# Performance work log

Hardware: AMD Instinct MI355X
Metric: run time of the kernel (lower is better)

The kernel has to match this reference:

```python
import jax, jax.numpy as jnp
import numpy as np

B, C, PC, P = 64, 32, 128, 2048
N = B * C * PC          # 262144 graph nodes
E = 2097152             # ~8 edges per node


def _gcn(x, src, dst, n, W, b):
    # PyG GCNConv: add self loops, sym-normalized mean aggregation of x@W
    xw = x @ W
    sl = jnp.arange(n, dtype=src.dtype)
    s = jnp.concatenate([src, sl]); d = jnp.concatenate([dst, sl])
    deg = jax.ops.segment_sum(jnp.ones(d.shape, xw.dtype), d, num_segments=n)
    dinv = jax.lax.rsqrt(deg)  # deg >= 1 thanks to self loops
    norm = dinv[s] * dinv[d]
    return jax.ops.segment_sum(xw[s] * norm[:, None], d, num_segments=n) + b


def _gat(x, src, dst, n, W, a_src, a_dst, b):
    # PyG GATConv (heads=1): self loops, edge softmax over incoming edges
    xw = x @ W
    sl = jnp.arange(n, dtype=src.dtype)
    s = jnp.concatenate([src, sl]); d = jnp.concatenate([dst, sl])
    e = jax.nn.leaky_relu((xw @ a_src)[s] + (xw @ a_dst)[d], 0.2)
    m = jax.ops.segment_max(jax.lax.stop_gradient(e), d, num_segments=n)
    ex = jnp.exp(e - m[d])
    denom = jax.ops.segment_sum(ex, d, num_segments=n)
    alpha = ex / denom[d]
    return jax.ops.segment_sum(xw[s] * alpha[:, None], d, num_segments=n) + b


def _cross_edges(num_cross, batch_size):
    # faithful to get_c_adjacency: every ordered pair (i!=j) appears twice per graph
    ii, jj = np.meshgrid(np.arange(num_cross), np.arange(num_cross), indexing='ij')
    m = ii != jj
    s, d = ii[m], jj[m]
    s2 = np.concatenate([s, d]); d2 = np.concatenate([d, s])
    off = (np.arange(batch_size) * num_cross)[:, None]
    src = (s2[None] + off).reshape(-1)
    dst = (d2[None] + off).reshape(-1)
    return jnp.asarray(src, jnp.int32), jnp.asarray(dst, jnp.int32)


def _conv1d(x, W, b):
    y = jax.lax.conv_general_dilated(x, W, (2,), ((1, 1),), dimension_numbers=('NCH', 'OIH', 'NCH'))
    return y + b[None, :, None]


def _bn_eval(x, gamma, beta):
    # BatchNorm1d in eval mode with default running stats (mean 0, var 1)
    scale = gamma / np.float32(np.sqrt(1.0 + 1e-5))
    return x * scale[None, :, None] + beta[None, :, None]


def setup_inputs() -> dict:
    key = jax.random.key(0)
    ks = jax.random.split(key, 32)
    rn = lambda k, sh, s=0.1: (jax.random.normal(k, sh, jnp.float32) * s)
    return {
        'x': jax.random.normal(ks[0], (N, 19), jnp.float32),
        'edge_index': jax.random.randint(ks[1], (2, E), 0, N, jnp.int32),
        'points': jax.random.normal(ks[2], (B, 3, P), jnp.float32),
        'W1': rn(ks[3], (19, 32)), 'b1': rn(ks[4], (32,)),
        'W2': rn(ks[5], (32, 64)), 'b2': rn(ks[6], (64,)),
        'W3': rn(ks[7], (64, 64)), 'b3': rn(ks[8], (64,)),
        'Wg1': rn(ks[9], (64, 64)), 'asrc1': rn(ks[10], (64,)), 'adst1': rn(ks[11], (64,)), 'bg1': rn(ks[12], (64,)),
        'Wg2': rn(ks[13], (64, 64)), 'asrc2': rn(ks[14], (64,)), 'adst2': rn(ks[15], (64,)), 'bg2': rn(ks[16], (64,)),
        'c1W': rn(ks[17], (32, 3, 3)), 'c1b': rn(ks[18], (32,)),
        'g1': 1.0 + rn(ks[19], (32,)), 'be1': rn(ks[20], (32,)),
        'c2W': rn(ks[21], (64, 32, 3)), 'c2b': rn(ks[22], (64,)),
        'g2': 1.0 + rn(ks[23], (64,)), 'be2': rn(ks[24], (64,)),
        'c3W': rn(ks[25], (64, 64, 3)), 'c3b': rn(ks[26], (64,)),
        'Wl2': rn(ks[27], (64, 64)), 'bl2': rn(ks[28], (64,)),
        'Wl3': rn(ks[29], (64, 1)), 'bl3': rn(ks[30], (1,)),
        'batch_size': B, 'num_cross': C, 'num_pieces': PC,
    }


def reference(x, edge_index, points, W1, b1, W2, b2, W3, b3,
              Wg1, asrc1, adst1, bg1, Wg2, asrc2, adst2, bg2,
              c1W, c1b, g1, be1, c2W, c2b, g2, be2, c3W, c3b,
              Wl2, bl2, Wl3, bl3, batch_size, num_cross, num_pieces):
    src, dst = edge_index[0], edge_index[1]
    n = x.shape[0]
    h = jax.nn.relu(_gcn(x, src, dst, n, W1, b1))  # dropout is a no-op in eval
    h = jax.nn.leaky_relu(_gcn(h, src, dst, n, W2, b2), 0.01)
    h = jax.nn.leaky_relu(_gcn(h, src, dst, n, W3, b3), 0.01)
    h = _gat(h, src, dst, n, Wg1, asrc1, adst1, bg1)
    h = h.reshape(batch_size, num_cross, num_pieces, -1).mean(-2)  # [B, C, 64]
    s2, d2 = _cross_edges(num_cross, batch_size)
    h = _gat(h.reshape(batch_size * num_cross, 64), s2, d2, batch_size * num_cross, Wg2, asrc2, adst2, bg2)
    h = h.reshape(batch_size, num_cross, 64).mean(1)  # [B, 64]
    p = _bn_eval(jax.nn.leaky_relu(_conv1d(points, c1W, c1b), 0.01), g1, be1)
    p = _bn_eval(jax.nn.leaky_relu(_conv1d(p, c2W, c2b), 0.01), g2, be2)
    p = jax.nn.leaky_relu(_conv1d(p, c3W, c3b), 0.01).mean(-1)  # AdaptiveAvgPool1d(1).squeeze -> [B, 64]
    h = h + p
    h = jax.nn.leaky_relu(h @ Wl2 + bl2, 0.01)
    return jax.nn.sigmoid(h @ Wl3 + bl3)  # [B, 1]
```

## Files before the change

### kernel.cpp

```cpp
#include <hip/hip_runtime.h>
#include <cstdint>
#include <cstddef>

#define NN 262144
#define EE 2097152
#define BB 64
#define CCROSS 32
#define PCC 128
#define PP 2048
#define NBUCK 256
#define BCAP 12288

typedef _Float16 f16;
typedef __attribute__((ext_vector_type(2))) _Float16 f16x2;
typedef __attribute__((ext_vector_type(4))) _Float16 f16x4;
typedef __attribute__((ext_vector_type(8))) _Float16 f16x8;
typedef __attribute__((ext_vector_type(4))) float f32x4;

static __device__ __forceinline__ float lrelu(float x, float s) { return x > 0.f ? x : s * x; }

#if __has_builtin(__builtin_amdgcn_fdot2)
static __device__ __forceinline__ float dot2f(unsigned x, unsigned w, float c) {
    return __builtin_amdgcn_fdot2(__builtin_bit_cast(f16x2, x), __builtin_bit_cast(f16x2, w), c, false);
}
#else
static __device__ __forceinline__ float dot2f(unsigned x, unsigned w, float c) {
    f16x2 a = __builtin_bit_cast(f16x2, x);
    f16x2 b = __builtin_bit_cast(f16x2, w);
    return fmaf((float)a[0], (float)b[0], fmaf((float)a[1], (float)b[1], c));
}
#endif

__global__ __launch_bounds__(256) void bucket_a_k(const int* __restrict__ src, const int* __restrict__ dst,
                                                  unsigned* __restrict__ buckets, int* __restrict__ gcnt) {
    __shared__ int hist[NBUCK];
    __shared__ int base[NBUCK];
    __shared__ unsigned short rankbuf[8192];
    const int tid = threadIdx.x;
    const int e0 = blockIdx.x * 8192;
    hist[tid] = 0;
    __syncthreads();
    for (int i = tid; i < 8192; i += 256) {
        int d = dst[e0 + i];
        rankbuf[i] = (unsigned short)atomicAdd(&hist[d >> 10], 1);
    }
    __syncthreads();
    base[tid] = tid * BCAP + atomicAdd(&gcnt[tid], hist[tid]);
    __syncthreads();
    for (int i = tid; i < 8192; i += 256) {
        int s = src[e0 + i];
        int d = dst[e0 + i];
        int b = d >> 10;
        buckets[base[b] + rankbuf[i]] = ((unsigned)s << 10) | (unsigned)(d & 1023);
    }
}

__global__ void bucket_scan_k(const int* __restrict__ gcnt, int* __restrict__ bbase, int* __restrict__ rp) {
    __shared__ int tmp[256];
    int tid = threadIdx.x;
    int v = gcnt[tid];
    tmp[tid] = v;
    __syncthreads();
    for (int off = 1; off < 256; off <<= 1) {
        int t = (tid >= off) ? tmp[tid - off] : 0;
        __syncthreads();
        tmp[tid] += t;
        __syncthreads();
    }
    bbase[tid] = tmp[tid] - v;
    if (tid == 0) rp[NN] = EE;
}

__global__ __launch_bounds__(256) void bucket_b_k(const unsigned* __restrict__ buckets, const int* __restrict__ gcnt,
                                                  const int* __restrict__ bbase, int* __restrict__ rp,
                                                  float* __restrict__ dinv, int* __restrict__ col) {
    __shared__ int cnt[1024];
    __shared__ int scan[1024];
    __shared__ int wsum[256];
    const int b = blockIdx.x;
    const int tid = threadIdx.x;
    int n = gcnt[b];
    if (n > BCAP) n = BCAP;
    const unsigned* eb = buckets + (size_t)b * BCAP;
    const int gb = bbase[b];
    for (int i = tid; i < 1024; i += 256) cnt[i] = 0;
    __syncthreads();
    for (int i = tid; i < n; i += 256) atomicAdd(&cnt[eb[i] & 1023], 1);
    __syncthreads();
    int b4 = tid * 4;
    int c0 = cnt[b4], c1 = cnt[b4 + 1], c2 = cnt[b4 + 2], c3 = cnt[b4 + 3];
    int tsum = c0 + c1 + c2 + c3;
    wsum[tid] = tsum;
    __syncthreads();
    for (int off = 1; off < 256; off <<= 1) {
        int t = (tid >= off) ? wsum[tid - off] : 0;
        __syncthreads();
        wsum[tid] += t;
        __syncthreads();
    }
    int excl = wsum[tid] - tsum;
    scan[b4] = excl;
    scan[b4 + 1] = excl + c0;
    scan[b4 + 2] = excl + c0 + c1;
    scan[b4 + 3] = excl + c0 + c1 + c2;
    int vbase = b * 1024 + b4;
    rp[vbase + 0] = gb + scan[b4 + 0];
    rp[vbase + 1] = gb + scan[b4 + 1];
    rp[vbase + 2] = gb + scan[b4 + 2];
    rp[vbase + 3] = gb + scan[b4 + 3];
    dinv[vbase + 0] = rsqrtf((float)(c0 + 1));
    dinv[vbase + 1] = rsqrtf((float)(c1 + 1));
    dinv[vbase + 2] = rsqrtf((float)(c2 + 1));
    dinv[vbase + 3] = rsqrtf((float)(c3 + 1));
    __syncthreads();
    for (int i = tid; i < 1024; i += 256) cnt[i] = 0;
    __syncthreads();
    for (int i = tid; i < n; i += 256) {
        unsigned p = eb[i];
        int dl = p & 1023;
        int r = atomicAdd(&cnt[dl], 1);
        col[gb + scan[dl] + r] = (int)(p >> 10);
    }
}

__global__ void zprep_k(const float* __restrict__ x, const float* __restrict__ dinv, f16* __restrict__ z) {
    int v = blockIdx.x * 256 + threadIdx.x;
    if (v >= NN) return;
    float dv = dinv[v];
    const float* xr = x + (size_t)v * 19;
    float vv[20];
#pragma unroll
    for (int k = 0; k < 19; k++) vv[k] = dv * xr[k];
    vv[19] = 0.f;
    f16x4* zr = (f16x4*)(z + (size_t)v * 32);
#pragma unroll
    for (int c = 0; c < 5; c++) {
        f16x4 t = {(f16)vv[4 * c], (f16)vv[4 * c + 1], (f16)vv[4 * c + 2], (f16)vv[4 * c + 3]};
        zr[c] = t;
    }
    f16x4 zz = {(f16)0.f, (f16)0.f, (f16)0.f, (f16)0.f};
#pragma unroll
    for (int c = 5; c < 8; c++) zr[c] = zz;
}

#define ZSTR1 36
template <int KINR, int KOUT, int ACT>
__global__ __launch_bounds__(256) void fused_agg_gemm_k(const f16* __restrict__ z, const int* __restrict__ rp,
                                                        const int* __restrict__ col, const float* __restrict__ Wg,
                                                        const float* __restrict__ dinv, const float* __restrict__ bias,
                                                        f16* __restrict__ zout) {
    constexpr int NO = KOUT / 4;
    __shared__ float Wl[32 * KOUT];
    __shared__ float zrow[64 * ZSTR1];
    const int tid = threadIdx.x;
    for (int i = tid; i < 32 * KOUT; i += 256) Wl[i] = (i < KINR * KOUT) ? Wg[i] : 0.f;

    const int r = tid >> 2;
    const int idx = tid & 3;
    const int v = blockIdx.x * 64 + r;
    const f16x8* z8 = (const f16x8*)z;
    f16x8 a = z8[(size_t)v * 4 + idx];
    float acc8[8];
#pragma unroll
    for (int j = 0; j < 8; j++) acc8[j] = (float)a[j];
    int st = rp[v], e = rp[v + 1];
    int i = st;
    for (; i + 4 <= e; i += 4) {
        int u0 = col[i], u1 = col[i + 1], u2 = col[i + 2], u3 = col[i + 3];
        f16x8 a0 = z8[(size_t)u0 * 4 + idx];
        f16x8 a1 = z8[(size_t)u1 * 4 + idx];
        f16x8 a2 = z8[(size_t)u2 * 4 + idx];
        f16x8 a3 = z8[(size_t)u3 * 4 + idx];
#pragma unroll
        for (int j = 0; j < 8; j++)
            acc8[j] += ((float)a0[j] + (float)a1[j]) + ((float)a2[j] + (float)a3[j]);
    }
    for (; i < e; i++) {
        f16x8 aa = z8[(size_t)col[i] * 4 + idx];
#pragma unroll
        for (int j = 0; j < 8; j++) acc8[j] += (float)aa[j];
    }
    float4 s0, s1;
    s0.x = acc8[0]; s0.y = acc8[1]; s0.z = acc8[2]; s0.w = acc8[3];
    s1.x = acc8[4]; s1.y = acc8[5]; s1.z = acc8[6]; s1.w = acc8[7];
    *(float4*)&zrow[r * ZSTR1 + idx * 8] = s0;
    *(float4*)&zrow[r * ZSTR1 + idx * 8 + 4] = s1;
    __syncthreads();

    float acc[NO];
#pragma unroll
    for (int j = 0; j < NO; j++) acc[j] = 0.f;
#pragma unroll 4
    for (int k = 0; k < 32; k++) {
        float zv = zrow[r * ZSTR1 + k];
        const float* wr = Wl + k * KOUT + NO * idx;
#pragma unroll
        for (int j = 0; j < NO; j++) acc[j] = fmaf(zv, wr[j], acc[j]);
    }
    float dv = dinv[v];
    f16 hv[NO];
#pragma unroll
    for (int j = 0; j < NO; j++) {
        float o = dv * acc[j] + bias[NO * idx + j];
        o = (ACT == 0) ? fmaxf(o, 0.f) : lrelu(o, 0.01f);
        hv[j] = (f16)(o * dv);
    }
    if constexpr (NO == 8) {
        f16x8 h = {hv[0], hv[1], hv[2], hv[3], hv[4], hv[5], hv[6], hv[7]};
        *(f16x8*)(zout + (size_t)v * KOUT + NO * idx) = h;
    } else {
        f16x8 h0 = {hv[0], hv[1], hv[2], hv[3], hv[4], hv[5], hv[6], hv[7]};
        f16x8 h1 = {hv[8], hv[9], hv[10], hv[11], hv[12], hv[13], hv[14], hv[15]};
        f16x8* yo = (f16x8*)(zout + (size_t)v * KOUT + NO * idx);
        yo[0] = h0; yo[1] = h1;
    }
}

__global__ __launch_bounds__(256) void agg_h16_k(const f16* __restrict__ y, const int* __restrict__ rp,
                                                 const int* __restrict__ col, f16* __restrict__ out) {
    int gid = blockIdx.x * 256 + threadIdx.x;
    int v = gid >> 3;
    int idx = gid & 7;
    const f16x8* y8 = (const f16x8*)y;
    f16x8 a = y8[(size_t)v * 8 + idx];
    float acc[8];
#pragma unroll
    for (int j = 0; j < 8; j++) acc[j] = (float)a[j];
    int s = rp[v], e = rp[v + 1];
    int i = s;
    for (; i + 4 <= e; i += 4) {
        int u0 = col[i], u1 = col[i + 1], u2 = col[i + 2], u3 = col[i + 3];
        f16x8 a0 = y8[(size_t)u0 * 8 + idx];
        f16x8 a1 = y8[(size_t)u1 * 8 + idx];
        f16x8 a2 = y8[(size_t)u2 * 8 + idx];
        f16x8 a3 = y8[(size_t)u3 * 8 + idx];
#pragma unroll
        for (int j = 0; j < 8; j++)
            acc[j] += ((float)a0[j] + (float)a1[j]) + ((float)a2[j] + (float)a3[j]);
    }
    for (; i < e; i++) {
        f16x8 aa = y8[(size_t)col[i] * 8 + idx];
#pragma unroll
        for (int j = 0; j < 8; j++) acc[j] += (float)aa[j];
    }
    f16x8 r;
#pragma unroll
    for (int j = 0; j < 8; j++) r[j] = (f16)acc[j];
    ((f16x8*)out)[(size_t)v * 8 + idx] = r;
}

__global__ void pack_w_k(const float* __restrict__ W, f16* __restrict__ out) {
    int o = blockIdx.x * 256 + threadIdx.x;
    if (o >= 4096) return;
    int frag = o >> 9;
    int kt = frag >> 2;
    int c = frag & 3;
    int idx = o & 511;
    int l = idx >> 3;
    int j = idx & 7;
    int k = kt * 32 + ((l >> 4) << 3) + j;
    int n = 16 * c + (l & 15);
    out[o] = (f16)W[k * 64 + n];
}

__global__ void pack_c2_k(const float* __restrict__ W, f16* __restrict__ out) {
    int o = blockIdx.x * 256 + threadIdx.x;
    if (o >= 64 * 96) return;
    int ch = o / 96, r = o - ch * 96;
    int k = r >> 5, ci = r & 31;
    out[o] = (f16)W[ch * 96 + ci * 3 + k];
}

__global__ void pack_c3_k(const float* __restrict__ W, f16* __restrict__ out) {
    int o = blockIdx.x * 256 + threadIdx.x;
    if (o >= 64 * 192) return;
    int ch = o / 192, r = o - ch * 192;
    int k = r >> 6, ci = r & 63;
    out[o] = (f16)W[ch * 192 + ci * 3 + k];
}

#define HSTR 72
__global__ __launch_bounds__(256) void gemm3_gat_k(const f16* __restrict__ aggz, const f16* __restrict__ w3p,
                                                   const float* __restrict__ dinv, const float* __restrict__ b3,
                                                   const f16* __restrict__ wgp, const float* __restrict__ av,
                                                   const float* __restrict__ ad, f16* __restrict__ xw,
                                                   float* __restrict__ es, float* __restrict__ ed) {
    __shared__ f16 zin[64 * HSTR];
    __shared__ f16 hh[64 * HSTR];
    const int tid = threadIdx.x;
    const int v0 = blockIdx.x * 64;
    {
        int row = tid >> 2;
        int kb = (tid & 3) * 16;
        const f16x8* zp = (const f16x8*)(aggz + (size_t)(v0 + row) * 64 + kb);
        f16x8 z0 = zp[0], z1 = zp[1];
        *(f16x8*)&zin[row * HSTR + kb] = z0;
        *(f16x8*)&zin[row * HSTR + kb + 8] = z1;
    }
    __syncthreads();

    const int w = tid >> 6;
    const int l = tid & 63;
    const int m = l & 15;
    const int q = l >> 4;
    const int r0 = 16 * w;

    f32x4 acc0 = {0.f, 0.f, 0.f, 0.f}, acc1 = acc0, acc2 = acc0, acc3 = acc0;
#pragma unroll
    for (int kt = 0; kt < 2; kt++) {
        f16x8 afrag = *(const f16x8*)&zin[(r0 + m) * HSTR + kt * 32 + q * 8];
        f16x8 b0 = *(const f16x8*)&w3p[((kt * 4 + 0) << 9) + l * 8];
        f16x8 b1 = *(const f16x8*)&w3p[((kt * 4 + 1) << 9) + l * 8];
        f16x8 b2 = *(const f16x8*)&w3p[((kt * 4 + 2) << 9) + l * 8];
        f16x8 b3f = *(const f16x8*)&w3p[((kt * 4 + 3) << 9) + l * 8];
        acc0 = __builtin_amdgcn_mfma_f32_16x16x32_f16(afrag, b0, acc0, 0, 0, 0);
        acc1 = __builtin_amdgcn_mfma_f32_16x16x32_f16(afrag, b1, acc1, 0, 0, 0);
        acc2 = __builtin_amdgcn_mfma_f32_16x16x32_f16(afrag, b2, acc2, 0, 0, 0);
        acc3 = __builtin_amdgcn_mfma_f32_16x16x32_f16(afrag, b3f, acc3, 0, 0, 0);
    }
    {
        float dv0 = dinv[v0 + r0 + q * 4 + 0];
        float dv1 = dinv[v0 + r0 + q * 4 + 1];
        float dv2 = dinv[v0 + r0 + q * 4 + 2];
        float dv3 = dinv[v0 + r0 + q * 4 + 3];
#pragma unroll
        for (int c = 0; c < 4; c++) {
            const f32x4* ac = (c == 0) ? &acc0 : (c == 1) ? &acc1 : (c == 2) ? &acc2 : &acc3;
            float bb = b3[16 * c + m];
            hh[(r0 + q * 4 + 0) * HSTR + 16 * c + m] = (f16)lrelu(dv0 * (*ac)[0] + bb, 0.01f);
            hh[(r0 + q * 4 + 1) * HSTR + 16 * c + m] = (f16)lrelu(dv1 * (*ac)[1] + bb, 0.01f);
            hh[(r0 + q * 4 + 2) * HSTR + 16 * c + m] = (f16)lrelu(dv2 * (*ac)[2] + bb, 0.01f);
            hh[(r0 + q * 4 + 3) * HSTR + 16 * c + m] = (f16)lrelu(dv3 * (*ac)[3] + bb, 0.01f);
        }
    }
    __syncthreads();

    acc0 = (f32x4){0.f, 0.f, 0.f, 0.f}; acc1 = acc0; acc2 = acc0; acc3 = acc0;
#pragma unroll
    for (int kt = 0; kt < 2; kt++) {
        f16x8 afrag = *(const f16x8*)&hh[(r0 + m) * HSTR + kt * 32 + q * 8];
        f16x8 b0 = *(const f16x8*)&wgp[((kt * 4 + 0) << 9) + l * 8];
        f16x8 b1 = *(const f16x8*)&wgp[((kt * 4 + 1) << 9) + l * 8];
        f16x8 b2 = *(const f16x8*)&wgp[((kt * 4 + 2) << 9) + l * 8];
        f16x8 b3f = *(const f16x8*)&wgp[((kt * 4 + 3) << 9) + l * 8];
        acc0 = __builtin_amdgcn_mfma_f32_16x16x32_f16(afrag, b0, acc0, 0, 0, 0);
        acc1 = __builtin_amdgcn_mfma_f32_16x16x32_f16(afrag, b1, acc1, 0, 0, 0);
        acc2 = __builtin_amdgcn_mfma_f32_16x16x32_f16(afrag, b2, acc2, 0, 0, 0);
        acc3 = __builtin_amdgcn_mfma_f32_16x16x32_f16(afrag, b3f, acc3, 0, 0, 0);
    }
    {
        float e1[4] = {0.f, 0.f, 0.f, 0.f}, e2[4] = {0.f, 0.f, 0.f, 0.f};
#pragma unroll
        for (int c = 0; c < 4; c++) {
            const f32x4* ac = (c == 0) ? &acc0 : (c == 1) ? &acc1 : (c == 2) ? &acc2 : &acc3;
            float a1 = av[16 * c + m];
            float d1 = ad[16 * c + m];
#pragma unroll
            for (int reg = 0; reg < 4; reg++) {
                float g = (*ac)[reg];
                e1[reg] = fmaf(g, a1, e1[reg]);
                e2[reg] = fmaf(g, d1, e2[reg]);
                xw[(size_t)(v0 + r0 + q * 4 + reg) * 64 + 16 * c + m] = (f16)g;
            }
        }
#pragma unroll
        for (int reg = 0; reg < 4; reg++) {
            e1[reg] += __shfl_xor(e1[reg], 1); e1[reg] += __shfl_xor(e1[reg], 2);
            e1[reg] += __shfl_xor(e1[reg], 4); e1[reg] += __shfl_xor(e1[reg], 8);
            e2[reg] += __shfl_xor(e2[reg], 1); e2[reg] += __shfl_xor(e2[reg], 2);
            e2[reg] += __shfl_xor(e2[reg], 4); e2[reg] += __shfl_xor(e2[reg], 8);
        }
        if (m == 0) {
#pragma unroll
            for (int reg = 0; reg < 4; reg++) {
                es[v0 + r0 + q * 4 + reg] = e1[reg];
                ed[v0 + r0 + q * 4 + reg] = e2[reg];
            }
        }
    }
}

__global__ void gat_w_k(const float* __restrict__ es, const float* __restrict__ ed,
                        const int* __restrict__ rp, const int* __restrict__ col,
                        f16* __restrict__ ew, float* __restrict__ wself, float* __restrict__ invden) {
    int v = blockIdx.x * 256 + threadIdx.x;
    if (v >= NN) return;
    float edv = ed[v];
    float eself = lrelu(es[v] + edv, 0.2f);
    float m = eself;
    int s = rp[v], e = rp[v + 1];
    int i = s;
    float lg[32];
    for (; i + 4 <= e; i += 4) {
        int u0 = col[i], u1 = col[i + 1], u2 = col[i + 2], u3 = col[i + 3];
        float t0 = lrelu(es[u0] + edv, 0.2f);
        float t1 = lrelu(es[u1] + edv, 0.2f);
        float t2 = lrelu(es[u2] + edv, 0.2f);
        float t3 = lrelu(es[u3] + edv, 0.2f);
        int k = i - s;
        if (k + 3 < 32) { lg[k] = t0; lg[k + 1] = t1; lg[k + 2] = t2; lg[k + 3] = t3; }
        m = fmaxf(m, fmaxf(fmaxf(t0, t1), fmaxf(t2, t3)));
    }
    for (; i < e; i++) {
        float t = lrelu(es[col[i]] + edv, 0.2f);
        int k = i - s;
        if (k < 32) lg[k] = t;
        m = fmaxf(m, t);
    }
    float wsl = __expf(eself - m);
    float den = wsl;
    for (i = s; i < e; i++) {
        int k = i - s;
        float t = (k < 32) ? lg[k] : lrelu(es[col[i]] + edv, 0.2f);
        float w = __expf(t - m);
        ew[i] = (f16)w;
        den += w;
    }
    wself[v] = wsl;
    invden[v] = 1.f / den;
}

__global__ __launch_bounds__(256) void gat_agg_pool_k(const f16* __restrict__ y, const int* __restrict__ rp,
                                                      const int* __restrict__ col, const f16* __restrict__ ew,
                                                      const float* __restrict__ wself, const float* __restrict__ invden,
                                                      const float* __restrict__ bias, float* __restrict__ pooled) {
    __shared__ float sred[32 * 68];
    const int g = blockIdx.x;
    const int tid = threadIdx.x;
    const int idx = tid & 7;
    const int slot = tid >> 3;
    const f16x8* y8 = (const f16x8*)y;
    float pacc[8];
#pragma unroll
    for (int j = 0; j < 8; j++) pacc[j] = 0.f;

#pragma unroll 1
    for (int pass = 0; pass < 4; pass++) {
        const int v = g * 128 + pass * 32 + slot;
        float ws = wself[v];
        f16x8 self = y8[(size_t)v * 8 + idx];
        float acc[8];
#pragma unroll
        for (int j = 0; j < 8; j++) acc[j] = ws * (float)self[j];
        int s = rp[v], e = rp[v + 1];
        int i = s;
        for (; i + 4 <= e; i += 4) {
            int u0 = col[i], u1 = col[i + 1], u2 = col[i + 2], u3 = col[i + 3];
            float w0 = (float)ew[i], w1 = (float)ew[i + 1], w2 = (float)ew[i + 2], w3 = (float)ew[i + 3];
            f16x8 a0 = y8[(size_t)u0 * 8 + idx];
            f16x8 a1 = y8[(size_t)u1 * 8 + idx];
            f16x8 a2 = y8[(size_t)u2 * 8 + idx];
            f16x8 a3 = y8[(size_t)u3 * 8 + idx];
#pragma unroll
            for (int j = 0; j < 8; j++)
                acc[j] = fmaf(w0, (float)a0[j], fmaf(w1, (float)a1[j], fmaf(w2, (float)a2[j], fmaf(w3, (float)a3[j], acc[j]))));
        }
        for (; i < e; i++) {
            float w = (float)ew[i];
            f16x8 aa = y8[(size_t)col[i] * 8 + idx];
#pragma unroll
            for (int j = 0; j < 8; j++) acc[j] = fmaf(w, (float)aa[j], acc[j]);
        }
        float inv = invden[v];
#pragma unroll
        for (int j = 0; j < 8; j++) pacc[j] = fmaf(acc[j], inv, pacc[j]);
    }

#pragma unroll
    for (int j = 0; j < 8; j++) sred[slot * 68 + idx * 8 + j] = pacc[j];
    __syncthreads();
    if (tid < 64) {
        float s = 0.f;
#pragma unroll
        for (int k = 0; k < 32; k++) s += sred[k * 68 + tid];
        pooled[(size_t)g * 64 + tid] = s * (1.f / 128.f) + bias[tid];
    }
}

__global__ void pool_cross_k(const float* __restrict__ in, float* __restrict__ out) {
    int gid = blockIdx.x * 64 + threadIdx.x;
    if (gid >= BB * 64) return;
    int f = gid & 63, b = gid >> 6;
    const float* p = in + (size_t)b * CCROSS * 64 + f;
    float s = 0.f;
#pragma unroll
    for (int i = 0; i < CCROSS; i++) s += p[(size_t)i * 64];
    out[gid] = s * (1.f / 32.f);
}

template <int KIN, int KOUT>
__global__ void gat_gemm_k(const float* __restrict__ x, const float* __restrict__ W,
                           float* __restrict__ y, const float* __restrict__ av, const float* __restrict__ ad,
                           float* __restrict__ es, float* __restrict__ ed, int n) {
    int v = blockIdx.x * 256 + threadIdx.x;
    if (v >= n) return;
    const float* xr = x + (size_t)v * KIN;
    float acc[KOUT];
#pragma unroll
    for (int j = 0; j < KOUT; j++) acc[j] = 0.f;
#pragma unroll 2
    for (int k = 0; k < KIN; k++) {
        float xv = xr[k];
#pragma unroll
        for (int j = 0; j < KOUT; j++) acc[j] = fmaf(xv, W[k * KOUT + j], acc[j]);
    }
    float e1 = 0.f, e2 = 0.f;
    float4* y4 = (float4*)(y + (size_t)v * KOUT);
#pragma unroll
    for (int j4 = 0; j4 < KOUT / 4; j4++) {
        float4 t;
        t.x = acc[4 * j4 + 0]; t.y = acc[4 * j4 + 1]; t.z = acc[4 * j4 + 2]; t.w = acc[4 * j4 + 3];
        y4[j4] = t;
        e1 = fmaf(t.x, av[4 * j4 + 0], e1); e1 = fmaf(t.y, av[4 * j4 + 1], e1);
        e1 = fmaf(t.z, av[4 * j4 + 2], e1); e1 = fmaf(t.w, av[4 * j4 + 3], e1);
        e2 = fmaf(t.x, ad[4 * j4 + 0], e2); e2 = fmaf(t.y, ad[4 * j4 + 1], e2);
        e2 = fmaf(t.z, ad[4 * j4 + 2], e2); e2 = fmaf(t.w, ad[4 * j4 + 3], e2);
    }
    es[v] = e1; ed[v] = e2;
}

__global__ void cross_att_k(const float* __restrict__ xw, const float* __restrict__ es,
                            const float* __restrict__ ed, const float* __restrict__ bg,
                            float* __restrict__ out) {
    int gid = blockIdx.x * 256 + threadIdx.x;
    if (gid >= BB * CCROSS * 64) return;
    int f = gid & 63;
    int d = (gid >> 6) & 31;
    int g = gid >> 11;
    int base = g * CCROSS;
    float edd = ed[base + d];
    float m = -1e30f;
#pragma unroll
    for (int s = 0; s < CCROSS; s++) {
        float e = lrelu(es[base + s] + edd, 0.2f);
        m = fmaxf(m, e);
    }
    float den = 0.f, acc = 0.f;
#pragma unroll
    for (int s = 0; s < CCROSS; s++) {
        float e = lrelu(es[base + s] + edd, 0.2f);
        float w = __expf(e - m) * ((s == d) ? 1.f : 2.f);
        den += w;
        acc = fmaf(w, xw[(size_t)(base + s) * 64 + f], acc);
    }
    out[gid] = acc / den + bg[f];
}

__global__ __launch_bounds__(256) void conv_fused_k(
        const float* __restrict__ pts, const float* __restrict__ c1W, const float* __restrict__ c1b,
        const float* __restrict__ g1, const float* __restrict__ be1,
        const f16* __restrict__ w2p, const float* __restrict__ c2b,
        const float* __restrict__ g2, const float* __restrict__ be2,
        const f16* __restrict__ w3pc, const float* __restrict__ c3b,
        float* __restrict__ partials) {
    __shared__ __align__(16) float s0[3 * 264];
    __shared__ __align__(16) f16 s1T[132 * 32];
    __shared__ __align__(16) f16 s2T[66 * 64];
    __shared__ float sred[256];

    const int b = blockIdx.x >> 3;
    const int q = blockIdx.x & 7;
    const int tid = threadIdx.x;
    const float bnscale = 0.99999500003749968f;

    const int lo0 = 256 * q - 7;
    for (int t = tid; t < 3 * 263; t += 256) {
        int c = t / 263, j = t - c * 263;
        int p = lo0 + j;
        s0[c * 264 + j] = (p >= 0 && p < PP) ? pts[((size_t)b * 3 + c) * PP + p] : 0.f;
    }
    __syncthreads();

    {
        const int ch = tid & 31;
        const int j0 = tid >> 5;
        float wv[9];
        const float* wg = c1W + ch * 9;
#pragma unroll
        for (int t = 0; t < 9; t++) wv[t] = wg[t];
        const float bs = c1b[ch];
        const float gs = g1[ch] * bnscale;
        const float bt = be1[ch];
        const int lo1 = 128 * q - 3;
        for (int j = j0; j < 131; j += 8) {
            int p1 = lo1 + j;
            float v = 0.f;
            if (p1 >= 0 && p1 < 1024) {
                const float* x0 = s0 + 2 * j;
                float a0 = bs, a1 = 0.f, a2 = 0.f;
#pragma unroll
                for (int c = 0; c < 3; c++) {
                    float2 x01 = *(const float2*)(x0 + c * 264);
                    float x2v = x0[c * 264 + 2];
                    a0 = fmaf(x01.x, wv[c * 3 + 0], a0);
                    a1 = fmaf(x01.y, wv[c * 3 + 1], a1);
                    a2 = fmaf(x2v, wv[c * 3 + 2], a2);
                }
                float acc = a0 + a1 + a2;
                acc = lrelu(acc, 0.01f);
                v = fmaf(acc, gs, bt);
            }
            s1T[j * 32 + ch] = (f16)v;
        }
    }
    __syncthreads();

    {
        const int ch = tid & 63;
        const int jg = tid >> 6;
        unsigned wr[48];
        const uint4* wp = (const uint4*)(w2p + (size_t)ch * 96);
#pragma unroll
        for (int t = 0; t < 12; t++) {
            uint4 u = wp[t];
            wr[4 * t + 0] = u.x; wr[4 * t + 1] = u.y; wr[4 * t + 2] = u.z; wr[4 * t + 3] = u.w;
        }
        const float bs = c2b[ch];
        const float gs = g2[ch] * bnscale;
        const float bt = be2[ch];
        const int lo2v = 64 * q - 1;
        for (int j = jg; j < 65; j += 4) {
            float ak[3] = {bs, 0.f, 0.f};
#pragma unroll
            for (int k = 0; k < 3; k++) {
                const uint4* xp = (const uint4*)(s1T + (2 * j + k) * 32);
                uint4 x0 = xp[0], x1 = xp[1], x2 = xp[2], x3 = xp[3];
                float a = ak[k];
                a = dot2f(x0.x, wr[k * 16 + 0], a);
                a = dot2f(x0.y, wr[k * 16 + 1], a);
                a = dot2f(x0.z, wr[k * 16 + 2], a);
                a = dot2f(x0.w, wr[k * 16 + 3], a);
                a = dot2f(x1.x, wr[k * 16 + 4], a);
                a = dot2f(x1.y, wr[k * 16 + 5], a);
                a = dot2f(x1.z, wr[k * 16 + 6], a);
                a = dot2f(x1.w, wr[k * 16 + 7], a);
                a = dot2f(x2.x, wr[k * 16 + 8], a);
                a = dot2f(x2.y, wr[k * 16 + 9], a);
                a = dot2f(x2.z, wr[k * 16 + 10], a);
                a = dot2f(x2.w, wr[k * 16 + 11], a);
                a = dot2f(x3.x, wr[k * 16 + 12], a);
                a = dot2f(x3.y, wr[k * 16 + 13], a);
                a = dot2f(x3.z, wr[k * 16 + 14], a);
                a = dot2f(x3.w, wr[k * 16 + 15], a);
                ak[k] = a;
            }
            float acc = ak[0] + ak[1] + ak[2];
            int p2 = lo2v + j;
            float v = 0.f;
            if (p2 >= 0 && p2 < 512) v = fmaf(lrelu(acc, 0.01f), gs, bt);
            s2T[j * 64 + ch] = (f16)v;
        }
    }
    __syncthreads();

    {
        const int ch = tid & 63;
        const int jg = tid >> 6;
        unsigned wr[96];
        const uint4* wp = (const uint4*)(w3pc + (size_t)ch * 192);
#pragma unroll
        for (int t = 0; t < 24; t++) {
            uint4 u = wp[t];
            wr[4 * t + 0] = u.x; wr[4 * t + 1] = u.y; wr[4 * t + 2] = u.z; wr[4 * t + 3] = u.w;
        }
        const float bs = c3b[ch];
        float psum = 0.f;
        for (int j = jg; j < 32; j += 4) {
            float ak[3] = {bs, 0.f, 0.f};
#pragma unroll
            for (int k = 0; k < 3; k++) {
                const uint4* xp = (const uint4*)(s2T + (2 * j + k) * 64);
                float a = ak[k];
#pragma unroll
                for (int t = 0; t < 8; t++) {
                    uint4 xv = xp[t];
                    a = dot2f(xv.x, wr[k * 32 + 4 * t + 0], a);
                    a = dot2f(xv.y, wr[k * 32 + 4 * t + 1], a);
                    a = dot2f(xv.z, wr[k * 32 + 4 * t + 2], a);
                    a = dot2f(xv.w, wr[k * 32 + 4 * t + 3], a);
                }
                ak[k] = a;
            }
            psum += lrelu(ak[0] + ak[1] + ak[2], 0.01f);
        }
        sred[tid] = psum;
    }
    __syncthreads();
    if (tid < 64) {
        float s = sred[tid] + sred[tid + 64] + sred[tid + 128] + sred[tid + 192];
        partials[((size_t)b * 8 + q) * 64 + tid] = s;
    }
}

__global__ void head_k(const float* __restrict__ hG, const float* __restrict__ partials,
                       const float* __restrict__ Wl2, const float* __restrict__ bl2,
                       const float* __restrict__ Wl3, const float* __restrict__ bl3,
                       float* __restrict__ out) {
    int b = blockIdx.x;
    int f = threadIdx.x;
    __shared__ float sh[64];
    float p = 0.f;
#pragma unroll
    for (int q = 0; q < 8; q++) p += partials[((size_t)b * 8 + q) * 64 + f];
    float h = hG[b * 64 + f] + p * (1.f / 256.f);
    sh[f] = h;
    __syncthreads();
    float acc = bl2[f];
#pragma unroll
    for (int k = 0; k < 64; k++) acc = fmaf(sh[k], Wl2[k * 64 + f], acc);
    acc = lrelu(acc, 0.01f);
    float pr = acc * Wl3[f];
#pragma unroll
    for (int off = 32; off > 0; off >>= 1) pr += __shfl_down(pr, off, 64);
    if (f == 0) out[b] = 1.f / (1.f + __expf(-(pr + bl3[0])));
}

extern "C" void kernel_launch(void* const* d_in, const int* in_sizes, int n_in,
                              void* d_out, int out_size, void* d_ws, size_t ws_size,
                              hipStream_t stream) {
    const float* x = (const float*)d_in[0];
    const int* ei = (const int*)d_in[1];
    const float* points = (const float*)d_in[2];
    const float* W1 = (const float*)d_in[3];
    const float* b1 = (const float*)d_in[4];
    const float* W2 = (const float*)d_in[5];
    const float* b2 = (const float*)d_in[6];
    const float* W3 = (const float*)d_in[7];
    const float* b3 = (const float*)d_in[8];
    const float* Wg1 = (const float*)d_in[9];
    const float* asrc1 = (const float*)d_in[10];
    const float* adst1 = (const float*)d_in[11];
    const float* bg1 = (const float*)d_in[12];
    const float* Wg2 = (const float*)d_in[13];
    const float* asrc2 = (const float*)d_in[14];
    const float* adst2 = (const float*)d_in[15];
    const float* bg2 = (const float*)d_in[16];
    const float* c1W = (const float*)d_in[17];
    const float* c1b = (const float*)d_in[18];
    const float* g1 = (const float*)d_in[19];
    const float* be1 = (const float*)d_in[20];
    const float* c2W = (const float*)d_in[21];
    const float* c2b = (const float*)d_in[22];
    const float* g2 = (const float*)d_in[23];
    const float* be2 = (const float*)d_in[24];
    const float* c3W = (const float*)d_in[25];
    const float* c3b = (const float*)d_in[26];
    const float* Wl2 = (const float*)d_in[27];
    const float* bl2 = (const float*)d_in[28];
    const float* Wl3 = (const float*)d_in[29];
    const float* bl3 = (const float*)d_in[30];

    const int* src = ei;
    const int* dst = ei + EE;

    char* w = (char*)d_ws;
    size_t off = 0;
    auto A = [&](size_t bytes) -> void* {
        void* p = w + off;
        off = (off + bytes + 255) & ~(size_t)255;
        return p;
    };
    int* colb = (int*)A((size_t)EE * 4);
    int* rp = (int*)A((size_t)(NN + 1) * 4);
    int* gcnt = (int*)A(NBUCK * 4);
    int* bbase = (int*)A(NBUCK * 4);
    float* dinv = (float*)A((size_t)NN * 4);
    float* bufA = (float*)A((size_t)NN * 64 * 4);
    f16* bufH1 = (f16*)A((size_t)NN * 64 * 2);
    f16* bufH2 = (f16*)A((size_t)NN * 64 * 2);
    f16* ew = (f16*)A((size_t)EE * 2);
    float* wself = (float*)A((size_t)NN * 4);
    float* invden = (float*)A((size_t)NN * 4);
    float* es = (float*)A((size_t)NN * 4);
    float* edv = (float*)A((size_t)NN * 4);
    f16* w3p = (f16*)A(4096 * 2);
    f16* wgp = (f16*)A(4096 * 2);
    f16* wc2p = (f16*)A(64 * 96 * 2);
    f16* wc3p = (f16*)A(64 * 192 * 2);
    float* pooled = (float*)A((size_t)BB * CCROSS * 64 * 4);
    float* xw2 = (float*)A((size_t)BB * CCROSS * 64 * 4);
    float* es2 = (float*)A((size_t)BB * CCROSS * 4);
    float* ed2 = (float*)A((size_t)BB * CCROSS * 4);
    float* crosso = (float*)A((size_t)BB * CCROSS * 64 * 4);
    float* hG = (float*)A((size_t)BB * 64 * 4);
    float* partials = (float*)A((size_t)BB * 8 * 64 * 4);

    unsigned* buckets = (unsigned*)bufA;
    f16* aggH = (f16*)bufA;

    hipMemsetAsync(gcnt, 0, NBUCK * 4, stream);
    bucket_a_k<<<EE / 8192, 256, 0, stream>>>(src, dst, buckets, gcnt);
    bucket_scan_k<<<1, 256, 0, stream>>>(gcnt, bbase, rp);
    bucket_b_k<<<NBUCK, 256, 0, stream>>>(buckets, gcnt, bbase, rp, dinv, colb);

    pack_c2_k<<<24, 256, 0, stream>>>(c2W, wc2p);
    pack_c3_k<<<48, 256, 0, stream>>>(c3W, wc3p);
    conv_fused_k<<<BB * 8, 256, 0, stream>>>(points, c1W, c1b, g1, be1, wc2p, c2b, g2, be2, wc3p, c3b, partials);
    pack_w_k<<<16, 256, 0, stream>>>(W3, w3p);
    pack_w_k<<<16, 256, 0, stream>>>(Wg1, wgp);

    zprep_k<<<NN / 256, 256, 0, stream>>>(x, dinv, bufH1);
    fused_agg_gemm_k<19, 32, 0><<<NN / 64, 256, 0, stream>>>(bufH1, rp, colb, W1, dinv, b1, bufH2);
    fused_agg_gemm_k<32, 64, 1><<<NN / 64, 256, 0, stream>>>(bufH2, rp, colb, W2, dinv, b2, bufH1);
    agg_h16_k<<<(NN * 8) / 256, 256, 0, stream>>>(bufH1, rp, colb, aggH);
    gemm3_gat_k<<<NN / 64, 256, 0, stream>>>(aggH, w3p, dinv, b3, wgp, asrc1, adst1,
                                             bufH2, es, edv);

    gat_w_k<<<NN / 256, 256, 0, stream>>>(es, edv, rp, colb, ew, wself, invden);
    gat_agg_pool_k<<<BB * CCROSS, 256, 0, stream>>>(bufH2, rp, colb, ew, wself, invden, bg1, pooled);

    gat_gemm_k<64, 64><<<(BB * CCROSS) / 256, 256, 0, stream>>>(pooled, Wg2, xw2, asrc2, adst2, es2, ed2, BB * CCROSS);
    cross_att_k<<<(BB * CCROSS * 64) / 256, 256, 0, stream>>>(xw2, es2, ed2, bg2, crosso);
    pool_cross_k<<<BB, 64, 0, stream>>>(crosso, hG);

    head_k<<<BB, 64, 0, stream>>>(hG, partials, Wl2, bl2, Wl3, bl3, (float*)d_out);
}
```

Measured before the change: 486.8 us.

## Fuse layer-3 aggregation into GEMM and flatten GAT pooling over CSR edges

Folds the standalone layer-3 neighbour aggregation into the gemm3_gat kernel, so each block gathers its 64 rows straight into shared memory. This removes an intermediate NN×64 half-precision write and read plus one kernel launch. GAT weights are now normalized by the softmax denominator inside gat_w_k. That lets gat_agg_pool_k walk the contiguous edge range of a whole 128-node group with strided threads instead of per-node loops, which balances load and removes the per-node invden multiply. The costs are fewer threads per row during the fused gather (4 rather than 8), which limits memory-level parallelism, and an extra pass over edges in gat_w_k.

```diff
diff --git a/kernel.cpp b/kernel.cpp
--- a/kernel.cpp
+++ b/kernel.cpp
@@ -216,39 +216,6 @@
     }
 }
 
-__global__ __launch_bounds__(256) void agg_h16_k(const f16* __restrict__ y, const int* __restrict__ rp,
-                                                 const int* __restrict__ col, f16* __restrict__ out) {
-    int gid = blockIdx.x * 256 + threadIdx.x;
-    int v = gid >> 3;
-    int idx = gid & 7;
-    const f16x8* y8 = (const f16x8*)y;
-    f16x8 a = y8[(size_t)v * 8 + idx];
-    float acc[8];
-#pragma unroll
-    for (int j = 0; j < 8; j++) acc[j] = (float)a[j];
-    int s = rp[v], e = rp[v + 1];
-    int i = s;
-    for (; i + 4 <= e; i += 4) {
-        int u0 = col[i], u1 = col[i + 1], u2 = col[i + 2], u3 = col[i + 3];
-        f16x8 a0 = y8[(size_t)u0 * 8 + idx];
-        f16x8 a1 = y8[(size_t)u1 * 8 + idx];
-        f16x8 a2 = y8[(size_t)u2 * 8 + idx];
-        f16x8 a3 = y8[(size_t)u3 * 8 + idx];
-#pragma unroll
-        for (int j = 0; j < 8; j++)
-            acc[j] += ((float)a0[j] + (float)a1[j]) + ((float)a2[j] + (float)a3[j]);
-    }
-    for (; i < e; i++) {
-        f16x8 aa = y8[(size_t)col[i] * 8 + idx];
-#pragma unroll
-        for (int j = 0; j < 8; j++) acc[j] += (float)aa[j];
-    }
-    f16x8 r;
-#pragma unroll
-    for (int j = 0; j < 8; j++) r[j] = (f16)acc[j];
-    ((f16x8*)out)[(size_t)v * 8 + idx] = r;
-}
-
 __global__ void pack_w_k(const float* __restrict__ W, f16* __restrict__ out) {
     int o = blockIdx.x * 256 + threadIdx.x;
     if (o >= 4096) return;
@@ -280,7 +247,8 @@
 }
 
 #define HSTR 72
-__global__ __launch_bounds__(256) void gemm3_gat_k(const f16* __restrict__ aggz, const f16* __restrict__ w3p,
+__global__ __launch_bounds__(256) void gemm3_gat_k(const f16* __restrict__ y, const int* __restrict__ rp,
+                                                   const int* __restrict__ col, const f16* __restrict__ w3p,
                                                    const float* __restrict__ dinv, const float* __restrict__ b3,
                                                    const f16* __restrict__ wgp, const float* __restrict__ av,
                                                    const float* __restrict__ ad, f16* __restrict__ xw,
@@ -290,12 +258,41 @@
     const int tid = threadIdx.x;
     const int v0 = blockIdx.x * 64;
     {
-        int row = tid >> 2;
-        int kb = (tid & 3) * 16;
-        const f16x8* zp = (const f16x8*)(aggz + (size_t)(v0 + row) * 64 + kb);
-        f16x8 z0 = zp[0], z1 = zp[1];
-        *(f16x8*)&zin[row * HSTR + kb] = z0;
-        *(f16x8*)&zin[row * HSTR + kb + 8] = z1;
+        const int row = tid >> 2;
+        const int idx = tid & 3;
+        const int v = v0 + row;
+        const f16x8* y8 = (const f16x8*)y;
+        f16x8 s0 = y8[(size_t)v * 8 + idx * 2];
+        f16x8 s1 = y8[(size_t)v * 8 + idx * 2 + 1];
+        float acc[16];
+#pragma unroll
+        for (int j = 0; j < 8; j++) { acc[j] = (float)s0[j]; acc[8 + j] = (float)s1[j]; }
+        int s = rp[v], e = rp[v + 1];
+        int i = s;
+        for (; i + 2 <= e; i += 2) {
+            int u0 = col[i], u1 = col[i + 1];
+            f16x8 a0 = y8[(size_t)u0 * 8 + idx * 2];
+            f16x8 a1 = y8[(size_t)u0 * 8 + idx * 2 + 1];
+            f16x8 b0 = y8[(size_t)u1 * 8 + idx * 2];
+            f16x8 b1 = y8[(size_t)u1 * 8 + idx * 2 + 1];
+#pragma unroll
+            for (int j = 0; j < 8; j++) {
+                acc[j] += (float)a0[j] + (float)b0[j];
+                acc[8 + j] += (float)a1[j] + (float)b1[j];
+            }
+        }
+        for (; i < e; i++) {
+            int u = col[i];
+            f16x8 a0 = y8[(size_t)u * 8 + idx * 2];
+            f16x8 a1 = y8[(size_t)u * 8 + idx * 2 + 1];
+#pragma unroll
+            for (int j = 0; j < 8; j++) { acc[j] += (float)a0[j]; acc[8 + j] += (float)a1[j]; }
+        }
+        f16x8 o0, o1;
+#pragma unroll
+        for (int j = 0; j < 8; j++) { o0[j] = (f16)acc[j]; o1[j] = (f16)acc[8 + j]; }
+        *(f16x8*)&zin[row * HSTR + idx * 16] = o0;
+        *(f16x8*)&zin[row * HSTR + idx * 16 + 8] = o1;
     }
     __syncthreads();
 
@@ -382,7 +379,7 @@
 
 __global__ void gat_w_k(const float* __restrict__ es, const float* __restrict__ ed,
                         const int* __restrict__ rp, const int* __restrict__ col,
-                        f16* __restrict__ ew, float* __restrict__ wself, float* __restrict__ invden) {
+                        f16* __restrict__ ewi, float* __restrict__ wsi) {
     int v = blockIdx.x * 256 + threadIdx.x;
     if (v >= NN) return;
     float edv = ed[v];
@@ -413,16 +410,21 @@
         int k = i - s;
         float t = (k < 32) ? lg[k] : lrelu(es[col[i]] + edv, 0.2f);
         float w = __expf(t - m);
-        ew[i] = (f16)w;
+        if (k < 32) lg[k] = w;
         den += w;
     }
-    wself[v] = wsl;
-    invden[v] = 1.f / den;
+    float inv = 1.f / den;
+    for (i = s; i < e; i++) {
+        int k = i - s;
+        float w = (k < 32) ? lg[k] : __expf(lrelu(es[col[i]] + edv, 0.2f) - m);
+        ewi[i] = (f16)(w * inv);
+    }
+    wsi[v] = wsl * inv;
 }
 
 __global__ __launch_bounds__(256) void gat_agg_pool_k(const f16* __restrict__ y, const int* __restrict__ rp,
-                                                      const int* __restrict__ col, const f16* __restrict__ ew,
-                                                      const float* __restrict__ wself, const float* __restrict__ invden,
+                                                      const int* __restrict__ col, const f16* __restrict__ ewi,
+                                                      const float* __restrict__ wsi,
                                                       const float* __restrict__ bias, float* __restrict__ pooled) {
     __shared__ float sred[32 * 68];
     const int g = blockIdx.x;
@@ -430,50 +432,49 @@
     const int idx = tid & 7;
     const int slot = tid >> 3;
     const f16x8* y8 = (const f16x8*)y;
-    float pacc[8];
-#pragma unroll
-    for (int j = 0; j < 8; j++) pacc[j] = 0.f;
-
-#pragma unroll 1
+    float acc[8];
+#pragma unroll
+    for (int j = 0; j < 8; j++) acc[j] = 0.f;
+
+#pragma unroll
     for (int pass = 0; pass < 4; pass++) {
         const int v = g * 128 + pass * 32 + slot;
-        float ws = wself[v];
+        float ws = wsi[v];
         f16x8 self = y8[(size_t)v * 8 + idx];
-        float acc[8];
-#pragma unroll
-        for (int j = 0; j < 8; j++) acc[j] = ws * (float)self[j];
-        int s = rp[v], e = rp[v + 1];
-        int i = s;
-        for (; i + 4 <= e; i += 4) {
-            int u0 = col[i], u1 = col[i + 1], u2 = col[i + 2], u3 = col[i + 3];
-            float w0 = (float)ew[i], w1 = (float)ew[i + 1], w2 = (float)ew[i + 2], w3 = (float)ew[i + 3];
-            f16x8 a0 = y8[(size_t)u0 * 8 + idx];
-            f16x8 a1 = y8[(size_t)u1 * 8 + idx];
-            f16x8 a2 = y8[(size_t)u2 * 8 + idx];
-            f16x8 a3 = y8[(size_t)u3 * 8 + idx];
-#pragma unroll
-            for (int j = 0; j < 8; j++)
-                acc[j] = fmaf(w0, (float)a0[j], fmaf(w1, (float)a1[j], fmaf(w2, (float)a2[j], fmaf(w3, (float)a3[j], acc[j]))));
-        }
-        for (; i < e; i++) {
-            float w = (float)ew[i];
-            f16x8 aa = y8[(size_t)col[i] * 8 + idx];
-#pragma unroll
-            for (int j = 0; j < 8; j++) acc[j] = fmaf(w, (float)aa[j], acc[j]);
-        }
-        float inv = invden[v];
-#pragma unroll
-        for (int j = 0; j < 8; j++) pacc[j] = fmaf(acc[j], inv, pacc[j]);
-    }
-
-#pragma unroll
-    for (int j = 0; j < 8; j++) sred[slot * 68 + idx * 8 + j] = pacc[j];
+#pragma unroll
+        for (int j = 0; j < 8; j++) acc[j] = fmaf(ws, (float)self[j], acc[j]);
+    }
+
+    const int s = rp[g * 128];
+    const int e = rp[g * 128 + 128];
+    int i = s + slot;
+    for (; i + 96 < e; i += 128) {
+        int u0 = col[i], u1 = col[i + 32], u2 = col[i + 64], u3 = col[i + 96];
+        float w0 = (float)ewi[i], w1 = (float)ewi[i + 32], w2 = (float)ewi[i + 64], w3 = (float)ewi[i + 96];
+        f16x8 a0 = y8[(size_t)u0 * 8 + idx];
+        f16x8 a1 = y8[(size_t)u1 * 8 + idx];
+        f16x8 a2 = y8[(size_t)u2 * 8 + idx];
+        f16x8 a3 = y8[(size_t)u3 * 8 + idx];
+#pragma unroll
+        for (int j = 0; j < 8; j++)
+            acc[j] = fmaf(w0, (float)a0[j], fmaf(w1, (float)a1[j], fmaf(w2, (float)a2[j], fmaf(w3, (float)a3[j], acc[j]))));
+    }
+    for (; i < e; i += 32) {
+        int u = col[i];
+        float w = (float)ewi[i];
+        f16x8 a = y8[(size_t)u * 8 + idx];
+#pragma unroll
+        for (int j = 0; j < 8; j++) acc[j] = fmaf(w, (float)a[j], acc[j]);
+    }
+
+#pragma unroll
+    for (int j = 0; j < 8; j++) sred[slot * 68 + idx * 8 + j] = acc[j];
     __syncthreads();
     if (tid < 64) {
-        float s = 0.f;
-#pragma unroll
-        for (int k = 0; k < 32; k++) s += sred[k * 68 + tid];
-        pooled[(size_t)g * 64 + tid] = s * (1.f / 128.f) + bias[tid];
+        float s2 = 0.f;
+#pragma unroll
+        for (int k = 0; k < 32; k++) s2 += sred[k * 68 + tid];
+        pooled[(size_t)g * 64 + tid] = s2 * (1.f / 128.f) + bias[tid];
     }
 }
 
@@ -768,9 +769,8 @@
     float* bufA = (float*)A((size_t)NN * 64 * 4);
     f16* bufH1 = (f16*)A((size_t)NN * 64 * 2);
     f16* bufH2 = (f16*)A((size_t)NN * 64 * 2);
-    f16* ew = (f16*)A((size_t)EE * 2);
-    float* wself = (float*)A((size_t)NN * 4);
-    float* invden = (float*)A((size_t)NN * 4);
+    f16* ewi = (f16*)A((size_t)EE * 2);
+    float* wsi = (float*)A((size_t)NN * 4);
     float* es = (float*)A((size_t)NN * 4);
     float* edv = (float*)A((size_t)NN * 4);
     f16* w3p = (f16*)A(4096 * 2);
@@ -786,7 +786,6 @@
     float* partials = (float*)A((size_t)BB * 8 * 64 * 4);
 
     unsigned* buckets = (unsigned*)bufA;
-    f16* aggH = (f16*)bufA;
 
     hipMemsetAsync(gcnt, 0, NBUCK * 4, stream);
     bucket_a_k<<<EE / 8192, 256, 0, stream>>>(src, dst, buckets, gcnt);
@@ -802,12 +801,11 @@
     zprep_k<<<NN / 256, 256, 0, stream>>>(x, dinv, bufH1);
     fused_agg_gemm_k<19, 32, 0><<<NN / 64, 256, 0, stream>>>(bufH1, rp, colb, W1, dinv, b1, bufH2);
     fused_agg_gemm_k<32, 64, 1><<<NN / 64, 256, 0, stream>>>(bufH2, rp, colb, W2, dinv, b2, bufH1);
-    agg_h16_k<<<(NN * 8) / 256, 256, 0, stream>>>(bufH1, rp, colb, aggH);
-    gemm3_gat_k<<<NN / 64, 256, 0, stream>>>(aggH, w3p, dinv, b3, wgp, asrc1, adst1,
+    gemm3_gat_k<<<NN / 64, 256, 0, stream>>>(bufH1, rp, colb, w3p, dinv, b3, wgp, asrc1, adst1,
                                              bufH2, es, edv);
 
-    gat_w_k<<<NN / 256, 256, 0, stream>>>(es, edv, rp, colb, ew, wself, invden);
-    gat_agg_pool_k<<<BB * CCROSS, 256, 0, stream>>>(bufH2, rp, colb, ew, wself, invden, bg1, pooled);
+    gat_w_k<<<NN / 256, 256, 0, stream>>>(es, edv, rp, colb, ewi, wsi);
+    gat_agg_pool_k<<<BB * CCROSS, 256, 0, stream>>>(bufH2, rp, colb, ewi, wsi, bg1, pooled);
 
     gat_gemm_k<64, 64><<<(BB * CCROSS) / 256, 256, 0, stream>>>(pooled, Wg2, xw2, asrc2, adst2, es2, ed2, BB * CCROSS);
     cross_att_k<<<(BB * CCROSS * 64) / 256, 256, 0, stream>>>(xw2, es2, ed2, bg2, crosso);
```

Result: faster. 473.8 us (-2.7%).
